# Performance work log

Hardware: AMD Instinct MI355X
Metric: run time of the kernel (lower is better)

The kernel has to match this reference:

```python
import jax, jax.numpy as jnp
import numpy as np

N_CAMP = 50
DAYS = 365          # execution_duration
N_STATES = 3
BASIS = 1e-10


def setup_inputs() -> dict:
    key = jax.random.key(0)
    k1, k2, k3, k4, k5 = jax.random.split(key, 5)
    adstock = jax.random.uniform(k1, (4096, N_CAMP, DAYS + 1), dtype=jnp.float32)
    mu = jax.random.normal(k2, (3,), dtype=jnp.float32)
    beta = jax.random.normal(k3, (3 * N_CAMP,), dtype=jnp.float32)
    init_prob = jax.random.normal(k4, (1,), dtype=jnp.float32)
    click_prob = jax.random.normal(k5, (1,), dtype=jnp.float32)
    return {"adstock": adstock, "mu": mu, "beta": beta,
            "init_prob": init_prob, "click_prob": click_prob}


def make_transition_matrix(mu, beta, adstock, basis=BASIS):
    b = adstock.shape[0]
    # [N_camp, 4]: zero column + reshaped betas
    beta_r = jnp.concatenate(
        [jnp.zeros((N_CAMP, 1), adstock.dtype), beta.reshape(N_CAMP, 3)], axis=1)
    # tensordot over campaign axis: [b, days, 4]
    O_beta = jnp.einsum('bcd,ck->bdk', adstock[:, :, 1:], beta_r)
    # [-inf, mu0, mu1, mu2]; exp(-inf)=0 kills the (0,0) slot exactly as in TF
    mu_full = jnp.concatenate([jnp.full((1,), -jnp.inf, dtype=mu.dtype), mu])
    mp = (mu_full[None, None, :] + O_beta).reshape(b, DAYS, N_STATES - 1, -1)
    num = jnp.exp(mp)                      # [b, D, 2, 2]
    den = 1.0 + jnp.sum(num, axis=3)       # [b, D, 2]
    main_diag = jnp.concatenate(
        [1.0 / den, jnp.ones((b, DAYS, 1), den.dtype)], axis=-1)   # [b, D, 3]
    lower_diag = jnp.concatenate(
        [num[:, :, 1:, 0] / den[:, :, 1:],
         jnp.zeros((b, DAYS, 1), den.dtype)], axis=-1)             # [b, D, 2]
    upper_diag = num[:, :, :, 1] / den                              # [b, D, 2]
    Q = jnp.zeros((b, DAYS, N_STATES, N_STATES), den.dtype)
    i = jnp.arange(N_STATES)
    Q = Q.at[..., i, i].set(main_diag)                 # main diagonal
    Q = Q.at[..., i[1:], i[:-1]].set(lower_diag)       # k = -1
    Q = Q.at[..., i[:-1], i[1:]].set(upper_diag)       # k = +1
    return jnp.maximum(Q, basis)


def reference(adstock, mu, beta, init_prob, click_prob):
    Q = make_transition_matrix(mu, beta, adstock)
    return Q, jax.nn.sigmoid(init_prob), jax.nn.sigmoid(click_prob)
```

## Files before the change

### kernel.cpp

```cpp
#include <hip/hip_runtime.h>

#define N_CAMP 50
#define DAYS   365
#define ROW    366
#define ROW2   (ROW / 2)
#define BASIS  1e-10f
#define BATCH  4096
#define NTHR   192

__global__ __launch_bounds__(NTHR)
void transition_prob_kernel(const float* __restrict__ adstock,
                            const float* __restrict__ mu,
                            const float* __restrict__ beta,
                            const float* __restrict__ init_prob,
                            const float* __restrict__ click_prob,
                            float* __restrict__ out)
{
    __shared__ float sb0[N_CAMP];
    __shared__ float sb1[N_CAMP];
    __shared__ float sb2[N_CAMP];
    __shared__ float smu[3];

    const int tid = threadIdx.x;
    const int b   = blockIdx.x;

    if (tid < 3 * N_CAMP) {
        const int c = tid / 3;
        const int k = tid % 3;
        const float v = beta[tid];
        if (k == 0) sb0[c] = v;
        else if (k == 1) sb1[c] = v;
        else sb2[c] = v;
    }
    if (tid < 3) smu[tid] = mu[tid];
    __syncthreads();

    if (b == 0 && tid == NTHR - 1) {
        const size_t base = (size_t)BATCH * DAYS * 9;
        out[base + 0] = 1.0f / (1.0f + __expf(-init_prob[0]));
        out[base + 1] = 1.0f / (1.0f + __expf(-click_prob[0]));
    }

    const int q = tid;
    if (q < ROW2) {
        const float2* arow = reinterpret_cast<const float2*>(
            adstock + (size_t)b * (N_CAMP * ROW)) + q;

        const float m0 = smu[0], m1 = smu[1], m2 = smu[2];

        float o1x = 0.f, o1y = 0.f;
        float o2x = 0.f, o2y = 0.f;
        float o3x = 0.f, o3y = 0.f;

#pragma unroll 10
        for (int c = 0; c < N_CAMP; ++c) {
            const float2 a = arow[c * ROW2];
            const float b0 = sb0[c], b1 = sb1[c], b2 = sb2[c];
            o1x = fmaf(a.x, b0, o1x); o1y = fmaf(a.y, b0, o1y);
            o2x = fmaf(a.x, b1, o2x); o2y = fmaf(a.y, b1, o2y);
            o3x = fmaf(a.x, b2, o3x); o3y = fmaf(a.y, b2, o3y);
        }

        {
            const float e1 = __expf(m0 + o1y);
            const float e2 = __expf(m1 + o2y);
            const float e3 = __expf(m2 + o3y);
            const float inv0 = __frcp_rn(1.0f + e1);
            const float inv1 = __frcp_rn(1.0f + e2 + e3);
            float* qo = out + ((size_t)b * DAYS + 2 * q) * 9;
            qo[0] = fmaxf(inv0,      BASIS);
            qo[1] = fmaxf(e1 * inv0, BASIS);
            qo[2] = BASIS;
            qo[3] = fmaxf(e2 * inv1, BASIS);
            qo[4] = fmaxf(inv1,      BASIS);
            qo[5] = fmaxf(e3 * inv1, BASIS);
            qo[6] = BASIS;
            qo[7] = BASIS;
            qo[8] = 1.0f;
        }
        if (q >= 1) {
            const float e1 = __expf(m0 + o1x);
            const float e2 = __expf(m1 + o2x);
            const float e3 = __expf(m2 + o3x);
            const float inv0 = __frcp_rn(1.0f + e1);
            const float inv1 = __frcp_rn(1.0f + e2 + e3);
            float* qo = out + ((size_t)b * DAYS + 2 * q - 1) * 9;
            qo[0] = fmaxf(inv0,      BASIS);
            qo[1] = fmaxf(e1 * inv0, BASIS);
            qo[2] = BASIS;
            qo[3] = fmaxf(e2 * inv1, BASIS);
            qo[4] = fmaxf(inv1,      BASIS);
            qo[5] = fmaxf(e3 * inv1, BASIS);
            qo[6] = BASIS;
            qo[7] = BASIS;
            qo[8] = 1.0f;
        }
    }
}

extern "C" void kernel_launch(void* const* d_in, const int* in_sizes, int n_in,
                              void* d_out, int out_size, void* d_ws, size_t ws_size,
                              hipStream_t stream)
{
    const float* adstock    = (const float*)d_in[0];
    const float* mu         = (const float*)d_in[1];
    const float* beta       = (const float*)d_in[2];
    const float* init_prob  = (const float*)d_in[3];
    const float* click_prob = (const float*)d_in[4];
    float* out = (float*)d_out;

    transition_prob_kernel<<<dim3(BATCH), dim3(NTHR), 0, stream>>>(
        adstock, mu, beta, init_prob, click_prob, out);
}
```

Before: 77.27 us.

## Stage adstock through shared memory with float4 loads, one day per thread

Each block now copies groups of 10 campaign rows into shared memory using float4 loads, then has 384 threads each accumulate one day from shared memory. Previously each thread read float2 pairs straight from global memory and handled two days. The aim is wider, fully coalesced global loads and more threads per block for latency hiding. The cost is extra syncthreads per group, a serialized load-then-compute phase with no double buffering, and more LDS use per block, which may lower occupancy. The float4 cast assumes the per-batch offset stays 16-byte aligned: 50*366 floats is a multiple of 4, and so is each 10-row group.

```diff
diff --git a/kernel.cpp b/kernel.cpp
--- a/kernel.cpp
+++ b/kernel.cpp
@@ -3,10 +3,12 @@
 #define N_CAMP 50
 #define DAYS   365
 #define ROW    366
-#define ROW2   (ROW / 2)
 #define BASIS  1e-10f
 #define BATCH  4096
-#define NTHR   192
+#define NTHR   384
+#define CPG    10
+#define NGROUP (N_CAMP / CPG)
+#define GROUP_F4 (CPG * ROW / 4)
 
 __global__ __launch_bounds__(NTHR)
 void transition_prob_kernel(const float* __restrict__ adstock,
@@ -16,6 +18,7 @@
                             const float* __restrict__ click_prob,
                             float* __restrict__ out)
 {
+    __shared__ float sA[CPG * ROW];
     __shared__ float sb0[N_CAMP];
     __shared__ float sb1[N_CAMP];
     __shared__ float sb2[N_CAMP];
@@ -33,7 +36,6 @@
         else sb2[c] = v;
     }
     if (tid < 3) smu[tid] = mu[tid];
-    __syncthreads();
 
     if (b == 0 && tid == NTHR - 1) {
         const size_t base = (size_t)BATCH * DAYS * 9;
@@ -41,60 +43,52 @@
         out[base + 1] = 1.0f / (1.0f + __expf(-click_prob[0]));
     }
 
-    const int q = tid;
-    if (q < ROW2) {
-        const float2* arow = reinterpret_cast<const float2*>(
-            adstock + (size_t)b * (N_CAMP * ROW)) + q;
+    const float4* rowbase = reinterpret_cast<const float4*>(
+        adstock + (size_t)b * (N_CAMP * ROW));
 
-        const float m0 = smu[0], m1 = smu[1], m2 = smu[2];
+    const int d = tid;
+    float o1 = 0.f, o2 = 0.f, o3 = 0.f;
 
-        float o1x = 0.f, o1y = 0.f;
-        float o2x = 0.f, o2y = 0.f;
-        float o3x = 0.f, o3y = 0.f;
+    for (int g = 0; g < NGROUP; ++g) {
+        __syncthreads();
 
-#pragma unroll 10
-        for (int c = 0; c < N_CAMP; ++c) {
-            const float2 a = arow[c * ROW2];
-            const float b0 = sb0[c], b1 = sb1[c], b2 = sb2[c];
-            o1x = fmaf(a.x, b0, o1x); o1y = fmaf(a.y, b0, o1y);
-            o2x = fmaf(a.x, b1, o2x); o2y = fmaf(a.y, b1, o2y);
-            o3x = fmaf(a.x, b2, o3x); o3y = fmaf(a.y, b2, o3y);
+        const float4* src = rowbase + g * GROUP_F4;
+        float4* dstv = reinterpret_cast<float4*>(sA);
+#pragma unroll
+        for (int i = tid; i < GROUP_F4; i += NTHR) {
+            dstv[i] = src[i];
         }
+        __syncthreads();
 
-        {
-            const float e1 = __expf(m0 + o1y);
-            const float e2 = __expf(m1 + o2y);
-            const float e3 = __expf(m2 + o3y);
-            const float inv0 = __frcp_rn(1.0f + e1);
-            const float inv1 = __frcp_rn(1.0f + e2 + e3);
-            float* qo = out + ((size_t)b * DAYS + 2 * q) * 9;
-            qo[0] = fmaxf(inv0,      BASIS);
-            qo[1] = fmaxf(e1 * inv0, BASIS);
-            qo[2] = BASIS;
-            qo[3] = fmaxf(e2 * inv1, BASIS);
-            qo[4] = fmaxf(inv1,      BASIS);
-            qo[5] = fmaxf(e3 * inv1, BASIS);
-            qo[6] = BASIS;
-            qo[7] = BASIS;
-            qo[8] = 1.0f;
+        if (d < DAYS) {
+            const int c0 = g * CPG;
+#pragma unroll
+            for (int cc = 0; cc < CPG; ++cc) {
+                const float a  = sA[cc * ROW + d + 1];
+                o1 = fmaf(a, sb0[c0 + cc], o1);
+                o2 = fmaf(a, sb1[c0 + cc], o2);
+                o3 = fmaf(a, sb2[c0 + cc], o3);
+            }
         }
-        if (q >= 1) {
-            const float e1 = __expf(m0 + o1x);
-            const float e2 = __expf(m1 + o2x);
-            const float e3 = __expf(m2 + o3x);
-            const float inv0 = __frcp_rn(1.0f + e1);
-            const float inv1 = __frcp_rn(1.0f + e2 + e3);
-            float* qo = out + ((size_t)b * DAYS + 2 * q - 1) * 9;
-            qo[0] = fmaxf(inv0,      BASIS);
-            qo[1] = fmaxf(e1 * inv0, BASIS);
-            qo[2] = BASIS;
-            qo[3] = fmaxf(e2 * inv1, BASIS);
-            qo[4] = fmaxf(inv1,      BASIS);
-            qo[5] = fmaxf(e3 * inv1, BASIS);
-            qo[6] = BASIS;
-            qo[7] = BASIS;
-            qo[8] = 1.0f;
-        }
+    }
+
+    if (d < DAYS) {
+        const float e1 = __expf(smu[0] + o1);
+        const float e2 = __expf(smu[1] + o2);
+        const float e3 = __expf(smu[2] + o3);
+        const float inv0 = __frcp_rn(1.0f + e1);
+        const float inv1 = __frcp_rn(1.0f + e2 + e3);
+
+        float* qo = out + ((size_t)b * DAYS + d) * 9;
+        qo[0] = fmaxf(inv0,      BASIS);
+        qo[1] = fmaxf(e1 * inv0, BASIS);
+        qo[2] = BASIS;
+        qo[3] = fmaxf(e2 * inv1, BASIS);
+        qo[4] = fmaxf(inv1,      BASIS);
+        qo[5] = fmaxf(e3 * inv1, BASIS);
+        qo[6] = BASIS;
+        qo[7] = BASIS;
+        qo[8] = 1.0f;
     }
 }
 
```

Measured after the change: 80.73 us. 4.5% more time.
